# Kernel tuning notes

Hardware: AMD Instinct MI355X
Metric: run time of the kernel (lower is better)

The kernel has to match this reference:

```python
import jax, jax.numpy as jnp
import numpy as np

SPATIAL_SCALE = 0.25
N, C, H, W = 8, 256, 128, 128
P = 100000
IMG = 512.0  # image-space extent (H / spatial_scale)


def setup_inputs() -> dict:
    key = jax.random.key(0)
    k1, k2, k3, k4 = jax.random.split(key, 4)
    features = jax.random.normal(k1, (N, C, H, W), dtype=jnp.float32)
    batch_idx = jax.random.randint(k2, (P,), 0, N).astype(jnp.float32)
    xy = jax.random.uniform(k3, (P, 2), dtype=jnp.float32) * IMG
    rois = jnp.concatenate([batch_idx[:, None], xy], axis=1)  # [P,3]: (b, x, y)
    return {"features": features, "rois": rois}


def _interp(features, rois, spatial_scale):
    n, c, h, w = features.shape
    b = rois[:, 0].astype(jnp.int32)
    x = rois[:, 1] * spatial_scale
    y = rois[:, 2] * spatial_scale
    # RoIAlign-style bilinear interpolation with boundary handling
    valid = (y >= -1.0) & (y <= h) & (x >= -1.0) & (x <= w)
    y = jnp.maximum(y, 0.0)
    x = jnp.maximum(x, 0.0)
    y_low = jnp.floor(y).astype(jnp.int32)
    x_low = jnp.floor(x).astype(jnp.int32)
    y_at_edge = y_low >= h - 1
    x_at_edge = x_low >= w - 1
    y_low = jnp.minimum(y_low, h - 1)
    x_low = jnp.minimum(x_low, w - 1)
    y_high = jnp.where(y_at_edge, y_low, y_low + 1)
    x_high = jnp.where(x_at_edge, x_low, x_low + 1)
    y = jnp.where(y_at_edge, y_low.astype(y.dtype), y)
    x = jnp.where(x_at_edge, x_low.astype(x.dtype), x)
    ly = y - y_low
    lx = x - x_low
    hy = 1.0 - ly
    hx = 1.0 - lx
    w1 = (hy * hx)[:, None]  # [P,1]
    w2 = (hy * lx)[:, None]
    w3 = (ly * hx)[:, None]
    w4 = (ly * lx)[:, None]
    # fancy-index gather: [P, C] per corner
    v1 = features[b, :, y_low, x_low]
    v2 = features[b, :, y_low, x_high]
    v3 = features[b, :, y_high, x_low]
    v4 = features[b, :, y_high, x_high]
    out = w1 * v1 + w2 * v2 + w3 * v3 + w4 * v4  # [P, C]
    return jnp.where(valid[:, None], out, 0.0)


def reference(features, rois):
    return _interp(features, rois, SPATIAL_SCALE)
```

## Files before the change

kernel.cpp:

```cpp
#include <hip/hip_runtime.h>

#define SCALE   0.25f
#define NBATCH  8
#define CCH     256
#define HH      128
#define WW      128
#define HW      (HH * WW)
#define NBUCK   (NBATCH * HH)
#define CAP     160

#define CG      32
#define NCG     (CCH / CG)

typedef float f32x4 __attribute__((ext_vector_type(4)));


__global__ __launch_bounds__(256) void k_bin(
    const float* __restrict__ rois, int* __restrict__ cnt,
    int4* __restrict__ slots, int P)
{
    __shared__ int lhist[NBUCK];
    __shared__ int lbase[NBUCK];
    const int t = threadIdx.x;
    for (int k = t; k < NBUCK; k += 256) lhist[k] = 0;
    __syncthreads();

    int p = blockIdx.x * 256 + t;
    int mybk = -1, mypos = 0;
    int4 myrec = make_int4(0, 0, 0, 0);
    if (p < P) {
        float fb = rois[3 * p];
        float fx = rois[3 * p + 1] * SCALE;
        float fy = rois[3 * p + 2] * SCALE;
        int b = (int)fb;
        bool valid = (fy >= -1.0f) && (fy <= (float)HH) &&
                     (fx >= -1.0f) && (fx <= (float)WW);
        float y = fmaxf(fy, 0.0f);
        float x = fmaxf(fx, 0.0f);
        int ylo = (int)floorf(y);
        int xlo = (int)floorf(x);
        float yf = y, xf = x;
        int xhi;
        if (ylo >= HH - 1) { ylo = HH - 1; yf = (float)ylo; }
        if (xlo >= WW - 1) { xlo = WW - 1; xhi = WW - 1; xf = (float)xlo; }
        else               { xhi = xlo + 1; }
        float ly = yf - (float)ylo;
        float lx = xf - (float)xlo;
        unsigned pk = (unsigned)xlo | ((unsigned)xhi << 8) | (valid ? 0u : 0x80000000u);
        int bk = b * HH + ylo;
        mybk  = bk;
        mypos = atomicAdd(&lhist[bk], 1);
        myrec = make_int4(p, (int)pk, __float_as_int(lx), __float_as_int(ly));
    }
    __syncthreads();
    for (int k = t; k < NBUCK; k += 256) {
        int h = lhist[k];
        lbase[k] = h ? atomicAdd(&cnt[k], h) : 0;
    }
    __syncthreads();
    if (mybk >= 0) {
        int idx = lbase[mybk] + mypos;
        if (idx < CAP) slots[mybk * CAP + idx] = myrec;
    }
}

__global__ __launch_bounds__(512, 6) void k_main(
    const float* __restrict__ feat, const int4* __restrict__ slots,
    const int* __restrict__ cnt_arr, float* __restrict__ out)
{
    const int bkp = blockIdx.x & 511;
    const int cgp = blockIdx.x >> 9;
    const int b   = bkp >> 6;
    const int y0  = (bkp & 63) * 2;
    const int bk0 = b * HH + y0;

    const int n0 = min(cnt_arr[bk0], CAP);
    const int n1 = min(cnt_arr[bk0 + 1], CAP);
    const int tot = n0 + n1;
    if (tot == 0) return;

    __shared__ __align__(16) float4 lds4[3][WW][8];

    const int t    = threadIdx.x;
    const int wv   = t >> 6;
    const int lane = t & 63;
    const int sub  = lane >> 3;
    const int cq   = lane & 7;

    const int4* sb = slots + (size_t)bk0 * CAP;
    const int ii0 = wv * 8;
    int j0 = min(ii0 + sub, tot - 1);        int q0 = j0 >= n0;
    int j1 = min(ii0 + 64 + sub, tot - 1);   int q1 = j1 >= n0;
    int j2 = min(ii0 + 128 + sub, tot - 1);  int q2 = j2 >= n0;
    int4 rc0 = sb[q0 ? CAP + j0 - n0 : j0];
    int4 rc1 = sb[q1 ? CAP + j1 - n0 : j1];
    int4 rc2 = sb[q2 ? CAP + j2 - n0 : j2];

    for (int u = t; u < 768; u += 512) {
        const int xq  = u & 31;
        const int cq8 = (u >> 5) & 7;
        const int row = u >> 8;
        const int y   = min(y0 + row, HH - 1);
        const float* g = feat + ((size_t)(b * CCH + cgp * CG + 4 * cq8) * HH + y) * WW + 4 * xq;
        float4 f0 = *(const float4*)(g);
        float4 f1 = *(const float4*)(g + HW);
        float4 f2 = *(const float4*)(g + 2 * HW);
        float4 f3 = *(const float4*)(g + 3 * HW);
        float4* d = &lds4[row][4 * xq][(cq8 + xq) & 7];
        d[0]  = make_float4(f0.x, f1.x, f2.x, f3.x);
        d[8]  = make_float4(f0.y, f1.y, f2.y, f3.y);
        d[16] = make_float4(f0.z, f1.z, f2.z, f3.z);
        d[24] = make_float4(f0.w, f1.w, f2.w, f3.w);
    }
    __syncthreads();

    float* const outbase = out + cgp * CG + 4 * cq;

    auto process = [&](int4 r, int q, bool act) {
        unsigned pk = (unsigned)r.y;
        float lx = __int_as_float(r.z);
        float ly = __int_as_float(r.w);
        float s  = ((int)pk < 0) ? 0.0f : 1.0f;
        float hy  = (1.0f - ly) * s;
        float lys = ly * s;
        float hx  = 1.0f - lx;
        float w1 = hy * hx, w2 = hy * lx, w3 = lys * hx, w4 = lys * lx;
        int xlo = pk & 255;
        int xhi = (pk >> 8) & 255;
        int alo = xlo * 8 + ((cq + (xlo >> 2)) & 7);
        int ahi = xhi * 8 + ((cq + (xhi >> 2)) & 7);
        const float4* lo = &lds4[q][0][0];
        const float4* hi = lo + WW * 8;
        float4 v1 = lo[alo], v2 = lo[ahi];
        float4 v3 = hi[alo], v4 = hi[ahi];
        f32x4 o;
        o.x = w1 * v1.x + w2 * v2.x + w3 * v3.x + w4 * v4.x;
        o.y = w1 * v1.y + w2 * v2.y + w3 * v3.y + w4 * v4.y;
        o.z = w1 * v1.z + w2 * v2.z + w3 * v3.z + w4 * v4.z;
        o.w = w1 * v1.w + w2 * v2.w + w3 * v3.w + w4 * v4.w;
        if (act)
            __builtin_nontemporal_store(o, (f32x4*)(outbase + (size_t)r.x * CCH));
    };

    process(rc0, q0, ii0 + sub < tot);
    if (ii0 + 64 < tot)  process(rc1, q1, ii0 + 64 + sub < tot);
    if (ii0 + 128 < tot) process(rc2, q2, ii0 + 128 + sub < tot);
    for (int ii = ii0 + 192; ii < tot; ii += 64) {
        int j = min(ii + sub, tot - 1);
        int q = j >= n0;
        process(sb[q ? CAP + j - n0 : j], q, ii + sub < tot);
    }
}

extern "C" void kernel_launch(void* const* d_in, const int* in_sizes, int n_in,
                              void* d_out, int out_size, void* d_ws, size_t ws_size,
                              hipStream_t stream) {
    const float* feat = (const float*)d_in[0];
    const float* rois = (const float*)d_in[1];
    float* out = (float*)d_out;
    const int P = in_sizes[1] / 3;

    int*  cnt   = (int*)d_ws;
    int4* slots = (int4*)((char*)d_ws + NBUCK * sizeof(int));

    hipMemsetAsync(cnt, 0, NBUCK * sizeof(int), stream);
    const int bb = (P + 255) / 256;
    k_bin<<<bb, 256, 0, stream>>>(rois, cnt, slots, P);
    k_main<<<NCG * NBATCH * (HH / 2), 512, 0, stream>>>(feat, slots, cnt, out);
}
```

Measured before the change: 242.5 us.

## Process row-pair buckets sequentially with two-row LDS buffer reuse

The kernel now stages two feature rows in LDS instead of three. It processes the first bucket's points, then overwrites one buffer with the third row and processes the second bucket with swapped lo/hi pointers. This cuts LDS per block from 48KB to 32KB and raises the launch-bounds occupancy hint from 6 to 8 blocks per CU. The cost is an extra __syncthreads and a serialized row load in the middle of each block. The early exit for empty bucket pairs is also removed, and the slot records are preloaded without clamping to the bucket counts.

```diff
diff --git a/kernel.cpp b/kernel.cpp
--- a/kernel.cpp
+++ b/kernel.cpp
@@ -11,6 +11,7 @@
 
 #define CG      32
 #define NCG     (CCH / CG)
+#define NPAIR   (NBATCH * HH / 2)
 
 typedef float f32x4 __attribute__((ext_vector_type(4)));
 
@@ -64,22 +65,17 @@
     }
 }
 
-__global__ __launch_bounds__(512, 6) void k_main(
+__global__ __launch_bounds__(512, 8) void k_main(
     const float* __restrict__ feat, const int4* __restrict__ slots,
     const int* __restrict__ cnt_arr, float* __restrict__ out)
 {
-    const int bkp = blockIdx.x & 511;
+    const int bkp = blockIdx.x & (NPAIR - 1);
     const int cgp = blockIdx.x >> 9;
     const int b   = bkp >> 6;
     const int y0  = (bkp & 63) * 2;
     const int bk0 = b * HH + y0;
 
-    const int n0 = min(cnt_arr[bk0], CAP);
-    const int n1 = min(cnt_arr[bk0 + 1], CAP);
-    const int tot = n0 + n1;
-    if (tot == 0) return;
-
-    __shared__ __align__(16) float4 lds4[3][WW][8];
+    __shared__ __align__(16) float4 lds4[2][WW][8];
 
     const int t    = threadIdx.x;
     const int wv   = t >> 6;
@@ -87,21 +83,22 @@
     const int sub  = lane >> 3;
     const int cq   = lane & 7;
 
+    const int c0 = min(cnt_arr[bk0], CAP);
+    const int c1 = min(cnt_arr[bk0 + 1], CAP);
+
     const int4* sb = slots + (size_t)bk0 * CAP;
     const int ii0 = wv * 8;
-    int j0 = min(ii0 + sub, tot - 1);        int q0 = j0 >= n0;
-    int j1 = min(ii0 + 64 + sub, tot - 1);   int q1 = j1 >= n0;
-    int j2 = min(ii0 + 128 + sub, tot - 1);  int q2 = j2 >= n0;
-    int4 rc0 = sb[q0 ? CAP + j0 - n0 : j0];
-    int4 rc1 = sb[q1 ? CAP + j1 - n0 : j1];
-    int4 rc2 = sb[q2 ? CAP + j2 - n0 : j2];
+    int4 ra0 = sb[ii0 + sub];
+    int4 ra1 = sb[ii0 + 64 + sub];
+    int4 rb0 = sb[CAP + ii0 + sub];
+    int4 rb1 = sb[CAP + ii0 + 64 + sub];
 
-    for (int u = t; u < 768; u += 512) {
-        const int xq  = u & 31;
-        const int cq8 = (u >> 5) & 7;
-        const int row = u >> 8;
-        const int y   = min(y0 + row, HH - 1);
-        const float* g = feat + ((size_t)(b * CCH + cgp * CG + 4 * cq8) * HH + y) * WW + 4 * xq;
+    {
+        const int xq  = t & 31;
+        const int cq8 = (t >> 5) & 7;
+        const int row = t >> 8;
+        const float* g = feat + (size_t)(b * CCH + cgp * CG + 4 * cq8) * HW
+                       + (y0 + row) * WW + 4 * xq;
         float4 f0 = *(const float4*)(g);
         float4 f1 = *(const float4*)(g + HW);
         float4 f2 = *(const float4*)(g + 2 * HW);
@@ -116,7 +113,7 @@
 
     float* const outbase = out + cgp * CG + 4 * cq;
 
-    auto process = [&](int4 r, int q, bool act) {
+    auto process = [&](int4 r, const float4* lo, const float4* hi, bool act) {
         unsigned pk = (unsigned)r.y;
         float lx = __int_as_float(r.z);
         float ly = __int_as_float(r.w);
@@ -125,12 +122,10 @@
         float lys = ly * s;
         float hx  = 1.0f - lx;
         float w1 = hy * hx, w2 = hy * lx, w3 = lys * hx, w4 = lys * lx;
-        int xlo = pk & 255;
-        int xhi = (pk >> 8) & 255;
+        int xlo = pk & 127;
+        int xhi = (pk >> 8) & 127;
         int alo = xlo * 8 + ((cq + (xlo >> 2)) & 7);
         int ahi = xhi * 8 + ((cq + (xhi >> 2)) & 7);
-        const float4* lo = &lds4[q][0][0];
-        const float4* hi = lo + WW * 8;
         float4 v1 = lo[alo], v2 = lo[ahi];
         float4 v3 = hi[alo], v4 = hi[ahi];
         f32x4 o;
@@ -142,13 +137,42 @@
             __builtin_nontemporal_store(o, (f32x4*)(outbase + (size_t)r.x * CCH));
     };
 
-    process(rc0, q0, ii0 + sub < tot);
-    if (ii0 + 64 < tot)  process(rc1, q1, ii0 + 64 + sub < tot);
-    if (ii0 + 128 < tot) process(rc2, q2, ii0 + 128 + sub < tot);
-    for (int ii = ii0 + 192; ii < tot; ii += 64) {
-        int j = min(ii + sub, tot - 1);
-        int q = j >= n0;
-        process(sb[q ? CAP + j - n0 : j], q, ii + sub < tot);
+    {
+        const float4* lo = &lds4[0][0][0];
+        const float4* hi = &lds4[1][0][0];
+        process(ra0, lo, hi, ii0 + sub < c0);
+        if (ii0 + 64 < c0) process(ra1, lo, hi, ii0 + 64 + sub < c0);
+        for (int ii = ii0 + 128; ii < c0; ii += 64)
+            process(sb[min(ii + sub, c0 - 1)], lo, hi, ii + sub < c0);
+    }
+    __syncthreads();
+
+    if (t < 256) {
+        const int xq  = t & 31;
+        const int cq8 = t >> 5;
+        const int y2  = min(y0 + 2, HH - 1);
+        const float* g = feat + (size_t)(b * CCH + cgp * CG + 4 * cq8) * HW
+                       + y2 * WW + 4 * xq;
+        float4 f0 = *(const float4*)(g);
+        float4 f1 = *(const float4*)(g + HW);
+        float4 f2 = *(const float4*)(g + 2 * HW);
+        float4 f3 = *(const float4*)(g + 3 * HW);
+        float4* d = &lds4[0][4 * xq][(cq8 + xq) & 7];
+        d[0]  = make_float4(f0.x, f1.x, f2.x, f3.x);
+        d[8]  = make_float4(f0.y, f1.y, f2.y, f3.y);
+        d[16] = make_float4(f0.z, f1.z, f2.z, f3.z);
+        d[24] = make_float4(f0.w, f1.w, f2.w, f3.w);
+    }
+    __syncthreads();
+
+    {
+        const float4* lo = &lds4[1][0][0];
+        const float4* hi = &lds4[0][0][0];
+        const int4* sb1 = sb + CAP;
+        process(rb0, lo, hi, ii0 + sub < c1);
+        if (ii0 + 64 < c1) process(rb1, lo, hi, ii0 + 64 + sub < c1);
+        for (int ii = ii0 + 128; ii < c1; ii += 64)
+            process(sb1[min(ii + sub, c1 - 1)], lo, hi, ii + sub < c1);
     }
 }
 
@@ -166,5 +190,5 @@
     hipMemsetAsync(cnt, 0, NBUCK * sizeof(int), stream);
     const int bb = (P + 255) / 256;
     k_bin<<<bb, 256, 0, stream>>>(rois, cnt, slots, P);
-    k_main<<<NCG * NBATCH * (HH / 2), 512, 0, stream>>>(feat, slots, cnt, out);
+    k_main<<<NCG * NPAIR, 512, 0, stream>>>(feat, slots, cnt, out);
 }
```

Result: no change. 244.2 us (+0.7%).
